# Performance work log

Measured on AMD Instinct MI355X. Metric: run time of the kernel, lower is better.

The kernel has to match this reference:

```python
import jax, jax.numpy as jnp
import numpy as np

WINDOW_SIZE = 11
SIGMA = 1.5
C1 = 0.01 ** 2
C2 = 0.03 ** 2


def _gaussian_window(window_size, channel):
    coords = jnp.arange(window_size, dtype=jnp.float32) - window_size // 2
    g = jnp.exp(-(coords ** 2) / (2.0 * SIGMA ** 2))
    g = g / g.sum()
    w2d = jnp.outer(g, g)  # [K, K]
    # depthwise conv kernel, OIHW with I=1 (feature_group_count=channel)
    return jnp.broadcast_to(w2d[None, None], (channel, 1, window_size, window_size))


def _depthwise_conv(x, window):
    pad = WINDOW_SIZE // 2
    return jax.lax.conv_general_dilated(
        x, window,
        window_strides=(1, 1),
        padding=((pad, pad), (pad, pad)),
        dimension_numbers=('NCHW', 'OIHW', 'NCHW'),
        feature_group_count=x.shape[1],
    )


def setup_inputs() -> dict:
    key = jax.random.key(0)
    k1, k2 = jax.random.split(key)
    shape = (32, 1, 512, 512)
    img1 = jax.random.uniform(k1, shape, dtype=jnp.float32)
    img2 = jax.random.uniform(k2, shape, dtype=jnp.float32)
    return {"img1": img1, "img2": img2}


def reference(img1, img2):
    channel = img1.shape[1]
    window = _gaussian_window(WINDOW_SIZE, channel).astype(img1.dtype)
    mu1 = _depthwise_conv(img1, window)
    mu2 = _depthwise_conv(img2, window)
    mu1_sq = mu1 * mu1
    mu2_sq = mu2 * mu2
    mu1_mu2 = mu1 * mu2
    sigma1_sq = _depthwise_conv(img1 * img1, window) - mu1_sq
    sigma2_sq = _depthwise_conv(img2 * img2, window) - mu2_sq
    sigma12 = _depthwise_conv(img1 * img2, window) - mu1_mu2
    ssim_map = ((2.0 * mu1_mu2 + C1) * (2.0 * sigma12 + C2)) / (
        (mu1_sq + mu2_sq + C1) * (sigma1_sq + sigma2_sq + C2))
    return 1.0 - ssim_map.mean()
```

## Files before the change

kernel.cpp:

```cpp
#include <hip/hip_runtime.h>

#define IMG   512
#define NIMG  32
#define TX    128
#define TY    16
#define NQ    36
#define VQS   17
#define VPL   (NQ * VQS)
#define VITEMS (NQ * 8)
#define NCH   4
#define NBX   (IMG / TX)
#define NBY   (IMG / TY)
#define NBLK  (NBX * NBY * NIMG)
#define NPIX  (32.0f * 512.0f * 512.0f)

constexpr float GW[11] = {
    0.00102838f, 0.00759876f, 0.03600077f, 0.10936069f, 0.21300553f,
    0.26601174f,
    0.21300553f, 0.10936069f, 0.03600077f, 0.00759876f, 0.00102838f
};
constexpr float C1c = 0.0001f;
constexpr float C2c = 0.0009f;

__global__ void ssim_init_out(float* __restrict__ out) { out[0] = 1.0f; }

__device__ __forceinline__ float4 f4mul(float4 a, float4 b) {
    return make_float4(a.x * b.x, a.y * b.y, a.z * b.z, a.w * b.w);
}
__device__ __forceinline__ float4 f4fma(float w, float4 v, float4 c) {
    return make_float4(fmaf(w, v.x, c.x), fmaf(w, v.y, c.y),
                       fmaf(w, v.z, c.z), fmaf(w, v.w, c.w));
}
__device__ __forceinline__ float4 f4fma_v(float4 a, float4 b, float4 c) {
    return make_float4(fmaf(a.x, b.x, c.x), fmaf(a.y, b.y, c.y),
                       fmaf(a.z, b.z, c.z), fmaf(a.w, b.w, c.w));
}

template <bool INTERIOR>
__device__ __forceinline__ void vpass_item(int it, int X0, int Y0,
        const float* __restrict__ a0, const float* __restrict__ b0,
        float4* __restrict__ sV4) {
    const int q  = it % NQ;
    const int g  = it / NQ;
    const int y0 = 2 * g;
    int gx0 = X0 - 8 + 4 * q;
    const int gyb = Y0 + y0 - 5;
    bool okx = true;
    if (!INTERIOR) {
        okx = (gx0 >= 0) && (gx0 + 3 < IMG);
        gx0 = min(max(gx0, 0), IMG - 4);
    }

    float4 ra[12], rb[12];
#pragma unroll
    for (int j = 0; j < 12; ++j) {
        int gy = gyb + j;
        if (!INTERIOR) gy = min(max(gy, 0), IMG - 1);
        const int off = gy * IMG + gx0;
        ra[j] = *(const float4*)(a0 + off);
        rb[j] = *(const float4*)(b0 + off);
    }

    float4 acc[NCH][2];
#pragma unroll
    for (int ch = 0; ch < NCH; ++ch)
#pragma unroll
        for (int o = 0; o < 2; ++o)
            acc[ch][o] = make_float4(0.f, 0.f, 0.f, 0.f);

#pragma unroll
    for (int k = 0; k < 12; ++k) {
        const float4 a  = ra[k];
        const float4 b  = rb[k];
        const float4 sq = f4fma_v(a, a, f4mul(b, b));
        const float4 ab = f4mul(a, b);
        if (INTERIOR) {
            if (k <= 10) {
                const float w = GW[k];
                acc[0][0] = f4fma(w, a,  acc[0][0]);
                acc[1][0] = f4fma(w, b,  acc[1][0]);
                acc[2][0] = f4fma(w, sq, acc[2][0]);
                acc[3][0] = f4fma(w, ab, acc[3][0]);
            }
            if (k >= 1) {
                const float w = GW[k - 1];
                acc[0][1] = f4fma(w, a,  acc[0][1]);
                acc[1][1] = f4fma(w, b,  acc[1][1]);
                acc[2][1] = f4fma(w, sq, acc[2][1]);
                acc[3][1] = f4fma(w, ab, acc[3][1]);
            }
        } else {
            const int gy = gyb + k;
            const bool ok = okx && ((unsigned)gy < IMG);
            float w0 = (k <= 10) ? GW[k] : 0.0f;
            float w1 = (k >= 1) ? GW[k - 1] : 0.0f;
            w0 = ok ? w0 : 0.0f;
            w1 = ok ? w1 : 0.0f;
            acc[0][0] = f4fma(w0, a,  acc[0][0]);
            acc[1][0] = f4fma(w0, b,  acc[1][0]);
            acc[2][0] = f4fma(w0, sq, acc[2][0]);
            acc[3][0] = f4fma(w0, ab, acc[3][0]);
            acc[0][1] = f4fma(w1, a,  acc[0][1]);
            acc[1][1] = f4fma(w1, b,  acc[1][1]);
            acc[2][1] = f4fma(w1, sq, acc[2][1]);
            acc[3][1] = f4fma(w1, ab, acc[3][1]);
        }
    }

#pragma unroll
    for (int o = 0; o < 2; ++o)
#pragma unroll
        for (int ch = 0; ch < NCH; ++ch)
            sV4[ch * VPL + q * VQS + (y0 + o)] = acc[ch][o];
}

__global__ __launch_bounds__(256, 4) void ssim_fused(
        const float* __restrict__ img1, const float* __restrict__ img2,
        float* __restrict__ ws, float* __restrict__ out) {
    __shared__ float4 sV4[NCH * VPL];

    const int tid = threadIdx.x;
    const int X0 = blockIdx.x * TX;
    const int Y0 = blockIdx.y * TY;
    const int n  = blockIdx.z;
    const float* a0 = img1 + (size_t)n * IMG * IMG;
    const float* b0 = img2 + (size_t)n * IMG * IMG;

    const bool interior = (X0 >= 8) && (X0 - 8 + 4 * (NQ - 1) + 3 < IMG) &&
                          (Y0 >= 5) && (Y0 + TY + 4 < IMG);

    if (interior) {
        for (int it = tid; it < VITEMS; it += 256)
            vpass_item<true>(it, X0, Y0, a0, b0, sV4);
    } else {
        for (int it = tid; it < VITEMS; it += 256)
            vpass_item<false>(it, X0, Y0, a0, b0, sV4);
    }
    __syncthreads();

    float sum = 0.0f;
    {
        const int y   = tid & 15;
        const int grp = tid >> 4;
        float res[NCH][8];
#pragma unroll
        for (int ch = 0; ch < NCH; ++ch) {
            const float4* base = &sV4[ch * VPL + y];
            float v[24];
#pragma unroll
            for (int d = 0; d < 6; ++d) {
                const float4 t = base[(2 * grp + d) * VQS];
                v[4 * d + 0] = t.x; v[4 * d + 1] = t.y;
                v[4 * d + 2] = t.z; v[4 * d + 3] = t.w;
            }
#pragma unroll
            for (int e = 0; e < 8; ++e) {
                float s = GW[0] * v[e + 3];
#pragma unroll
                for (int k = 1; k < 11; ++k) s = fmaf(GW[k], v[e + 3 + k], s);
                res[ch][e] = s;
            }
        }
#pragma unroll
        for (int e = 0; e < 8; ++e) {
            const float mu1 = res[0][e], mu2 = res[1][e];
            const float m1s = mu1 * mu1;
            const float m2s = mu2 * mu2;
            const float m12 = mu1 * mu2;
            const float msum = m1s + m2s;
            const float ssum = res[2][e] - msum;
            const float s12  = res[3][e] - m12;
            const float num = (2.0f * m12 + C1c) * (2.0f * s12 + C2c);
            const float den = (msum + C1c) * (ssum + C2c);
            sum += num * __builtin_amdgcn_rcpf(den);
        }
    }

#pragma unroll
    for (int off = 32; off > 0; off >>= 1)
        sum += __shfl_down(sum, off, 64);

    __shared__ float wred[4];
    if ((tid & 63) == 0) wred[tid >> 6] = sum;
    __syncthreads();
    if (tid == 0) {
        const float s = wred[0] + wred[1] + wred[2] + wred[3];
        if (ws) {
            const int bid = blockIdx.x +
                (int)gridDim.x * (blockIdx.y + (int)gridDim.y * blockIdx.z);
            ws[bid] = s;
        } else {
            atomicAdd(out, -s * (1.0f / NPIX));
        }
    }
}

__global__ __launch_bounds__(1024) void ssim_reduce(
        const float* __restrict__ ws, float* __restrict__ out) {
    const int t = threadIdx.x;
    float s = 0.0f;
    for (int i = t; i < NBLK; i += 1024) s += ws[i];
#pragma unroll
    for (int off = 32; off > 0; off >>= 1)
        s += __shfl_down(s, off, 64);
    __shared__ float wr[16];
    if ((t & 63) == 0) wr[t >> 6] = s;
    __syncthreads();
    if (t < 64) {
        float v = (t < 16) ? wr[t] : 0.0f;
#pragma unroll
        for (int off = 8; off > 0; off >>= 1)
            v += __shfl_down(v, off, 64);
        if (t == 0) out[0] = 1.0f - v * (1.0f / NPIX);
    }
}

extern "C" void kernel_launch(void* const* d_in, const int* in_sizes, int n_in,
                              void* d_out, int out_size, void* d_ws, size_t ws_size,
                              hipStream_t stream) {
    const float* img1 = (const float*)d_in[0];
    const float* img2 = (const float*)d_in[1];
    float* out = (float*)d_out;
    const bool two_stage = (d_ws != nullptr) && (ws_size >= NBLK * sizeof(float));
    float* ws = two_stage ? (float*)d_ws : nullptr;

    if (!two_stage) ssim_init_out<<<1, 1, 0, stream>>>(out);

    dim3 grid(NBX, NBY, NIMG);
    ssim_fused<<<grid, 256, 0, stream>>>(img1, img2, ws, out);

    if (two_stage) ssim_reduce<<<1, 1024, 0, stream>>>(ws, out);
}
```

Baseline: 117.2 us.

## Split fused SSIM into two channel-pair passes to halve LDS and raise occupancy

The vertical and horizontal convolution stages now run twice per block: first for the two means, then for the summed squares and the cross product. Each pass handles only two channels, so the shared buffer is halved and fewer registers are live. Launch bounds go from 4 to 8 waves' worth of blocks per CU to exploit this. In exchange, each block loads its image tile from global memory twice and adds an extra barrier round, and the mean results must stay in registers across the second pass.

```diff
diff --git a/kernel.cpp b/kernel.cpp
--- a/kernel.cpp
+++ b/kernel.cpp
@@ -8,7 +8,6 @@
 #define VQS   17
 #define VPL   (NQ * VQS)
 #define VITEMS (NQ * 8)
-#define NCH   4
 #define NBX   (IMG / TX)
 #define NBY   (IMG / TY)
 #define NBLK  (NBX * NBY * NIMG)
@@ -36,7 +35,7 @@
                        fmaf(a.z, b.z, c.z), fmaf(a.w, b.w, c.w));
 }
 
-template <bool INTERIOR>
+template <bool INTERIOR, int GROUP>
 __device__ __forceinline__ void vpass_item(int it, int X0, int Y0,
         const float* __restrict__ a0, const float* __restrict__ b0,
         float4* __restrict__ sV4) {
@@ -51,73 +50,86 @@
         gx0 = min(max(gx0, 0), IMG - 4);
     }
 
-    float4 ra[12], rb[12];
-#pragma unroll
-    for (int j = 0; j < 12; ++j) {
-        int gy = gyb + j;
+    float4 acc[2][2];
+#pragma unroll
+    for (int ch = 0; ch < 2; ++ch)
+#pragma unroll
+        for (int o = 0; o < 2; ++o)
+            acc[ch][o] = make_float4(0.f, 0.f, 0.f, 0.f);
+
+#pragma unroll
+    for (int k = 0; k < 12; ++k) {
+        int gy = gyb + k;
         if (!INTERIOR) gy = min(max(gy, 0), IMG - 1);
         const int off = gy * IMG + gx0;
-        ra[j] = *(const float4*)(a0 + off);
-        rb[j] = *(const float4*)(b0 + off);
-    }
-
-    float4 acc[NCH][2];
-#pragma unroll
-    for (int ch = 0; ch < NCH; ++ch)
-#pragma unroll
-        for (int o = 0; o < 2; ++o)
-            acc[ch][o] = make_float4(0.f, 0.f, 0.f, 0.f);
-
-#pragma unroll
-    for (int k = 0; k < 12; ++k) {
-        const float4 a  = ra[k];
-        const float4 b  = rb[k];
-        const float4 sq = f4fma_v(a, a, f4mul(b, b));
-        const float4 ab = f4mul(a, b);
+        const float4 a = *(const float4*)(a0 + off);
+        const float4 b = *(const float4*)(b0 + off);
+        float4 c0, c1;
+        if (GROUP == 0) {
+            c0 = a;
+            c1 = b;
+        } else {
+            c0 = f4fma_v(a, a, f4mul(b, b));
+            c1 = f4mul(a, b);
+        }
         if (INTERIOR) {
             if (k <= 10) {
                 const float w = GW[k];
-                acc[0][0] = f4fma(w, a,  acc[0][0]);
-                acc[1][0] = f4fma(w, b,  acc[1][0]);
-                acc[2][0] = f4fma(w, sq, acc[2][0]);
-                acc[3][0] = f4fma(w, ab, acc[3][0]);
+                acc[0][0] = f4fma(w, c0, acc[0][0]);
+                acc[1][0] = f4fma(w, c1, acc[1][0]);
             }
             if (k >= 1) {
                 const float w = GW[k - 1];
-                acc[0][1] = f4fma(w, a,  acc[0][1]);
-                acc[1][1] = f4fma(w, b,  acc[1][1]);
-                acc[2][1] = f4fma(w, sq, acc[2][1]);
-                acc[3][1] = f4fma(w, ab, acc[3][1]);
+                acc[0][1] = f4fma(w, c0, acc[0][1]);
+                acc[1][1] = f4fma(w, c1, acc[1][1]);
             }
         } else {
-            const int gy = gyb + k;
-            const bool ok = okx && ((unsigned)gy < IMG);
+            const int gyr = gyb + k;
+            const bool ok = okx && ((unsigned)gyr < IMG);
             float w0 = (k <= 10) ? GW[k] : 0.0f;
             float w1 = (k >= 1) ? GW[k - 1] : 0.0f;
             w0 = ok ? w0 : 0.0f;
             w1 = ok ? w1 : 0.0f;
-            acc[0][0] = f4fma(w0, a,  acc[0][0]);
-            acc[1][0] = f4fma(w0, b,  acc[1][0]);
-            acc[2][0] = f4fma(w0, sq, acc[2][0]);
-            acc[3][0] = f4fma(w0, ab, acc[3][0]);
-            acc[0][1] = f4fma(w1, a,  acc[0][1]);
-            acc[1][1] = f4fma(w1, b,  acc[1][1]);
-            acc[2][1] = f4fma(w1, sq, acc[2][1]);
-            acc[3][1] = f4fma(w1, ab, acc[3][1]);
+            acc[0][0] = f4fma(w0, c0, acc[0][0]);
+            acc[1][0] = f4fma(w0, c1, acc[1][0]);
+            acc[0][1] = f4fma(w1, c0, acc[0][1]);
+            acc[1][1] = f4fma(w1, c1, acc[1][1]);
         }
     }
 
 #pragma unroll
     for (int o = 0; o < 2; ++o)
 #pragma unroll
-        for (int ch = 0; ch < NCH; ++ch)
+        for (int ch = 0; ch < 2; ++ch)
             sV4[ch * VPL + q * VQS + (y0 + o)] = acc[ch][o];
 }
 
-__global__ __launch_bounds__(256, 4) void ssim_fused(
+__device__ __forceinline__ void hpass2(const float4* __restrict__ sV4,
+        int y, int grp, float res[2][8]) {
+#pragma unroll
+    for (int ch = 0; ch < 2; ++ch) {
+        const float4* base = &sV4[ch * VPL + y];
+        float v[24];
+#pragma unroll
+        for (int d = 0; d < 6; ++d) {
+            const float4 t = base[(2 * grp + d) * VQS];
+            v[4 * d + 0] = t.x; v[4 * d + 1] = t.y;
+            v[4 * d + 2] = t.z; v[4 * d + 3] = t.w;
+        }
+#pragma unroll
+        for (int e = 0; e < 8; ++e) {
+            float s = GW[0] * v[e + 3];
+#pragma unroll
+            for (int k = 1; k < 11; ++k) s = fmaf(GW[k], v[e + 3 + k], s);
+            res[ch][e] = s;
+        }
+    }
+}
+
+__global__ __launch_bounds__(256, 8) void ssim_fused(
         const float* __restrict__ img1, const float* __restrict__ img2,
         float* __restrict__ ws, float* __restrict__ out) {
-    __shared__ float4 sV4[NCH * VPL];
+    __shared__ float4 sV4[2 * VPL];
 
     const int tid = threadIdx.x;
     const int X0 = blockIdx.x * TX;
@@ -129,51 +141,47 @@
     const bool interior = (X0 >= 8) && (X0 - 8 + 4 * (NQ - 1) + 3 < IMG) &&
                           (Y0 >= 5) && (Y0 + TY + 4 < IMG);
 
+    const int y   = tid & 15;
+    const int grp = tid >> 4;
+
     if (interior) {
         for (int it = tid; it < VITEMS; it += 256)
-            vpass_item<true>(it, X0, Y0, a0, b0, sV4);
+            vpass_item<true, 0>(it, X0, Y0, a0, b0, sV4);
     } else {
         for (int it = tid; it < VITEMS; it += 256)
-            vpass_item<false>(it, X0, Y0, a0, b0, sV4);
-    }
-    __syncthreads();
+            vpass_item<false, 0>(it, X0, Y0, a0, b0, sV4);
+    }
+    __syncthreads();
+
+    float mu[2][8];
+    hpass2(sV4, y, grp, mu);
+    __syncthreads();
+
+    if (interior) {
+        for (int it = tid; it < VITEMS; it += 256)
+            vpass_item<true, 1>(it, X0, Y0, a0, b0, sV4);
+    } else {
+        for (int it = tid; it < VITEMS; it += 256)
+            vpass_item<false, 1>(it, X0, Y0, a0, b0, sV4);
+    }
+    __syncthreads();
+
+    float st[2][8];
+    hpass2(sV4, y, grp, st);
 
     float sum = 0.0f;
-    {
-        const int y   = tid & 15;
-        const int grp = tid >> 4;
-        float res[NCH][8];
-#pragma unroll
-        for (int ch = 0; ch < NCH; ++ch) {
-            const float4* base = &sV4[ch * VPL + y];
-            float v[24];
-#pragma unroll
-            for (int d = 0; d < 6; ++d) {
-                const float4 t = base[(2 * grp + d) * VQS];
-                v[4 * d + 0] = t.x; v[4 * d + 1] = t.y;
-                v[4 * d + 2] = t.z; v[4 * d + 3] = t.w;
-            }
-#pragma unroll
-            for (int e = 0; e < 8; ++e) {
-                float s = GW[0] * v[e + 3];
-#pragma unroll
-                for (int k = 1; k < 11; ++k) s = fmaf(GW[k], v[e + 3 + k], s);
-                res[ch][e] = s;
-            }
-        }
-#pragma unroll
-        for (int e = 0; e < 8; ++e) {
-            const float mu1 = res[0][e], mu2 = res[1][e];
-            const float m1s = mu1 * mu1;
-            const float m2s = mu2 * mu2;
-            const float m12 = mu1 * mu2;
-            const float msum = m1s + m2s;
-            const float ssum = res[2][e] - msum;
-            const float s12  = res[3][e] - m12;
-            const float num = (2.0f * m12 + C1c) * (2.0f * s12 + C2c);
-            const float den = (msum + C1c) * (ssum + C2c);
-            sum += num * __builtin_amdgcn_rcpf(den);
-        }
+#pragma unroll
+    for (int e = 0; e < 8; ++e) {
+        const float mu1 = mu[0][e], mu2 = mu[1][e];
+        const float m1s = mu1 * mu1;
+        const float m2s = mu2 * mu2;
+        const float m12 = mu1 * mu2;
+        const float msum = m1s + m2s;
+        const float ssum = st[0][e] - msum;
+        const float s12  = st[1][e] - m12;
+        const float num = (2.0f * m12 + C1c) * (2.0f * s12 + C2c);
+        const float den = (msum + C1c) * (ssum + C2c);
+        sum += num * __builtin_amdgcn_rcpf(den);
     }
 
 #pragma unroll
```

After: 292.8 us. 150% more time.

## Halve tile height, interleave channel smem layout, raise occupancy to 8 blocks

Applied to the files above, without the earlier changes.

Reduces the tile height from 16 to 8 rows so each thread does one vertical-pass item, and streams loads directly instead of buffering 12 rows of float4 in registers. The shared buffer is reorganised so all four channels for a column quad sit together with a padded stride of 33. Launch bounds are raised to 8 blocks per CU to hide latency. In exchange, the vertical halo overhead relative to tile height roughly doubles global reads, and the horizontal pass does 4 outputs per thread instead of 8.

```diff
diff --git a/kernel.cpp b/kernel.cpp
--- a/kernel.cpp
+++ b/kernel.cpp
@@ -3,12 +3,10 @@
 #define IMG   512
 #define NIMG  32
 #define TX    128
-#define TY    16
+#define TY    8
 #define NQ    36
-#define VQS   17
-#define VPL   (NQ * VQS)
-#define VITEMS (NQ * 8)
-#define NCH   4
+#define SSTR  33
+#define VITEMS (NQ * TY / 2)
 #define NBX   (IMG / TX)
 #define NBY   (IMG / TY)
 #define NBLK  (NBX * NBY * NIMG)
@@ -51,27 +49,20 @@
         gx0 = min(max(gx0, 0), IMG - 4);
     }
 
-    float4 ra[12], rb[12];
-#pragma unroll
-    for (int j = 0; j < 12; ++j) {
-        int gy = gyb + j;
+    float4 acc[4][2];
+#pragma unroll
+    for (int ch = 0; ch < 4; ++ch)
+#pragma unroll
+        for (int o = 0; o < 2; ++o)
+            acc[ch][o] = make_float4(0.f, 0.f, 0.f, 0.f);
+
+#pragma unroll
+    for (int k = 0; k < 12; ++k) {
+        int gy = gyb + k;
         if (!INTERIOR) gy = min(max(gy, 0), IMG - 1);
         const int off = gy * IMG + gx0;
-        ra[j] = *(const float4*)(a0 + off);
-        rb[j] = *(const float4*)(b0 + off);
-    }
-
-    float4 acc[NCH][2];
-#pragma unroll
-    for (int ch = 0; ch < NCH; ++ch)
-#pragma unroll
-        for (int o = 0; o < 2; ++o)
-            acc[ch][o] = make_float4(0.f, 0.f, 0.f, 0.f);
-
-#pragma unroll
-    for (int k = 0; k < 12; ++k) {
-        const float4 a  = ra[k];
-        const float4 b  = rb[k];
+        const float4 a  = *(const float4*)(a0 + off);
+        const float4 b  = *(const float4*)(b0 + off);
         const float4 sq = f4fma_v(a, a, f4mul(b, b));
         const float4 ab = f4mul(a, b);
         if (INTERIOR) {
@@ -90,8 +81,8 @@
                 acc[3][1] = f4fma(w, ab, acc[3][1]);
             }
         } else {
-            const int gy = gyb + k;
-            const bool ok = okx && ((unsigned)gy < IMG);
+            const int gyr = gyb + k;
+            const bool ok = okx && ((unsigned)gyr < IMG);
             float w0 = (k <= 10) ? GW[k] : 0.0f;
             float w1 = (k >= 1) ? GW[k - 1] : 0.0f;
             w0 = ok ? w0 : 0.0f;
@@ -110,14 +101,14 @@
 #pragma unroll
     for (int o = 0; o < 2; ++o)
 #pragma unroll
-        for (int ch = 0; ch < NCH; ++ch)
-            sV4[ch * VPL + q * VQS + (y0 + o)] = acc[ch][o];
-}
-
-__global__ __launch_bounds__(256, 4) void ssim_fused(
+        for (int ch = 0; ch < 4; ++ch)
+            sV4[q * SSTR + ch * TY + (y0 + o)] = acc[ch][o];
+}
+
+__global__ __launch_bounds__(256, 8) void ssim_fused(
         const float* __restrict__ img1, const float* __restrict__ img2,
         float* __restrict__ ws, float* __restrict__ out) {
-    __shared__ float4 sV4[NCH * VPL];
+    __shared__ float4 sV4[NQ * SSTR];
 
     const int tid = threadIdx.x;
     const int X0 = blockIdx.x * TX;
@@ -129,32 +120,29 @@
     const bool interior = (X0 >= 8) && (X0 - 8 + 4 * (NQ - 1) + 3 < IMG) &&
                           (Y0 >= 5) && (Y0 + TY + 4 < IMG);
 
-    if (interior) {
-        for (int it = tid; it < VITEMS; it += 256)
-            vpass_item<true>(it, X0, Y0, a0, b0, sV4);
-    } else {
-        for (int it = tid; it < VITEMS; it += 256)
-            vpass_item<false>(it, X0, Y0, a0, b0, sV4);
+    if (tid < VITEMS) {
+        if (interior) vpass_item<true>(tid, X0, Y0, a0, b0, sV4);
+        else          vpass_item<false>(tid, X0, Y0, a0, b0, sV4);
     }
     __syncthreads();
 
     float sum = 0.0f;
     {
-        const int y   = tid & 15;
-        const int grp = tid >> 4;
-        float res[NCH][8];
-#pragma unroll
-        for (int ch = 0; ch < NCH; ++ch) {
-            const float4* base = &sV4[ch * VPL + y];
-            float v[24];
-#pragma unroll
-            for (int d = 0; d < 6; ++d) {
-                const float4 t = base[(2 * grp + d) * VQS];
+        const int y = tid & 7;
+        const int G = tid >> 3;
+        float res[4][4];
+#pragma unroll
+        for (int ch = 0; ch < 4; ++ch) {
+            const float4* base = &sV4[ch * TY + y];
+            float v[20];
+#pragma unroll
+            for (int d = 0; d < 5; ++d) {
+                const float4 t = base[(G + d) * SSTR];
                 v[4 * d + 0] = t.x; v[4 * d + 1] = t.y;
                 v[4 * d + 2] = t.z; v[4 * d + 3] = t.w;
             }
 #pragma unroll
-            for (int e = 0; e < 8; ++e) {
+            for (int e = 0; e < 4; ++e) {
                 float s = GW[0] * v[e + 3];
 #pragma unroll
                 for (int k = 1; k < 11; ++k) s = fmaf(GW[k], v[e + 3 + k], s);
@@ -162,7 +150,7 @@
             }
         }
 #pragma unroll
-        for (int e = 0; e < 8; ++e) {
+        for (int e = 0; e < 4; ++e) {
             const float mu1 = res[0][e], mu2 = res[1][e];
             const float m1s = mu1 * mu1;
             const float m2s = mu2 * mu2;
```

Measured after the change: 419.3 us. +257.8%, slower.
